# Kernel tuning notes

Hardware: AMD Instinct MI355X
Metric: run time of the kernel (lower is better)

Reference implementation:

```python
import jax, jax.numpy as jnp
import numpy as np

VOCAB, EMB, HID, B, T = 50000, 16, 32, 4096, 500


def setup_inputs() -> dict:
    key = jax.random.key(0)
    k1, k2, k3, k4 = jax.random.split(key, 4)
    tokens = jax.random.randint(k1, (B, T), 0, VOCAB, dtype=jnp.int32)
    emb_table = jax.random.normal(k2, (VOCAB, EMB), dtype=jnp.float32) * 0.05
    kernel = jax.random.normal(k3, (EMB, 4 * HID), dtype=jnp.float32) * (1.0 / np.sqrt(EMB))
    rec_kernel = jax.random.normal(k4, (HID, 4 * HID), dtype=jnp.float32) * (1.0 / np.sqrt(HID))
    # Keras default: unit_forget_bias=True -> forget-gate bias = 1
    bias = jnp.concatenate([
        jnp.zeros((HID,), jnp.float32),
        jnp.ones((HID,), jnp.float32),
        jnp.zeros((2 * HID,), jnp.float32),
    ])
    return {"tokens": tokens, "emb_table": emb_table, "kernel": kernel,
            "rec_kernel": rec_kernel, "bias": bias}


def reference(tokens, emb_table, kernel, rec_kernel, bias):
    # Embedding with mask_zero=True: mask = tokens != 0
    embedded = emb_table[tokens]                 # [B, T, EMB]
    mask = (tokens != 0)                         # [B, T] bool
    # Precompute input projections for all timesteps (one big GEMM)
    x_proj = jnp.einsum('bte,eh->bth', embedded, kernel) + bias  # [B, T, 4H]

    def step(carry, xs):
        h, c = carry                              # [B, H] each
        xp_t, m_t = xs                            # [B, 4H], [B]
        z = xp_t + h @ rec_kernel                 # [B, 4H]
        i, f, g, o = jnp.split(z, 4, axis=-1)     # Keras gate order i,f,c,o
        i = jax.nn.sigmoid(i)
        f = jax.nn.sigmoid(f)
        g = jnp.tanh(g)
        o = jax.nn.sigmoid(o)
        c_new = f * c + i * g
        h_new = o * jnp.tanh(c_new)
        m = m_t[:, None]
        # masked steps carry previous state through (Keras LSTM mask semantics)
        h = jnp.where(m, h_new, h)
        c = jnp.where(m, c_new, c)
        return (h, c), None

    h0 = jnp.zeros((tokens.shape[0], HID), jnp.float32)
    c0 = jnp.zeros((tokens.shape[0], HID), jnp.float32)
    xs = (jnp.swapaxes(x_proj, 0, 1), jnp.swapaxes(mask, 0, 1))  # time-major
    (h, c), _ = jax.lax.scan(step, (h0, c0), xs)
    return h                                      # [B, HID] last (masked) output
```

## Files before the change

kernel.cpp:

```cpp
#include <hip/hip_runtime.h>
#include <cstdint>

#define VOCAB_N 50000
#define EMB_N   16
#define HID_N   32
#define B_N     4096
#define T_N     500

typedef __attribute__((ext_vector_type(8))) short bf16x8;
typedef __attribute__((ext_vector_type(4))) float f32x4;

__device__ __forceinline__ float frcp(float x) { return __builtin_amdgcn_rcpf(x); }
__device__ __forceinline__ float sigm(float x) {
  return frcp(1.0f + exp2f(x * -1.4426950408889634f));
}
__device__ __forceinline__ float tanh_fast(float x) {
  return fmaf(-2.0f, frcp(1.0f + exp2f(x * 2.8853900817779268f)), 1.0f);
}

__device__ __forceinline__ unsigned bf16_split_pack(float x) {
  unsigned u  = __builtin_bit_cast(unsigned, x);
  float hif = __builtin_bit_cast(float, u & 0xFFFF0000u);
  float r   = x - hif;
  unsigned lo = __builtin_bit_cast(unsigned, r) >> 16;
  return (u >> 16) | (lo << 16);
}

__global__ void build_proj_mfma(const float* __restrict__ emb,
                                const float* __restrict__ W,
                                const float* __restrict__ bias,
                                float* __restrict__ proj) {
  __shared__ float Wl[EMB_N * 128];
  __shared__ float bl[128];
  const int tid = threadIdx.x;
  for (int i = tid; i < EMB_N * 128 / 4; i += 256)
    reinterpret_cast<float4*>(Wl)[i] = reinterpret_cast<const float4*>(W)[i];
  if (tid < 32)
    reinterpret_cast<float4*>(bl)[tid] = reinterpret_cast<const float4*>(bias)[tid];
  __syncthreads();

  const long long gid = (long long)blockIdx.x * 256 + tid;
  if (gid >= (long long)VOCAB_N * 128) return;
  const int v = (int)(gid >> 7);
  const int q = (int)(gid & 127);
  const int c = q >> 3, n = q & 7;
  const int col = n * 16 + c;

  const float4* ev = reinterpret_cast<const float4*>(emb + (size_t)v * EMB_N);
  float4 e0 = ev[0], e1 = ev[1], e2 = ev[2], e3 = ev[3];
  const float em[16] = {e0.x,e0.y,e0.z,e0.w, e1.x,e1.y,e1.z,e1.w,
                        e2.x,e2.y,e2.z,e2.w, e3.x,e3.y,e3.z,e3.w};
  float a = bl[col];
#pragma unroll
  for (int e = 0; e < EMB_N; ++e) a = fmaf(em[e], Wl[e * 128 + col], a);
  proj[gid] = a;
}

#define SPLIT8(VAL, IDX)                                                      \
  { unsigned s_ = bf16_split_pack(VAL);                                       \
    Ah[IDX] = (short)s_; Al[IDX] = (short)(s_ >> 16); }

#define LSTM_MSTEP(TOKC, TOKP, XP0, XP1)                                      \
  {                                                                           \
                \
    float4 hv0 = *reinterpret_cast<const float4*>(&hl[c16][g8]);              \
    float4 hv1 = *reinterpret_cast<const float4*>(&hl[c16][g8 + 4]);          \
    bf16x8 Ah, Al;                                                            \
    SPLIT8(hv0.x, 0) SPLIT8(hv0.y, 1) SPLIT8(hv0.z, 2) SPLIT8(hv0.w, 3)      \
    SPLIT8(hv1.x, 4) SPLIT8(hv1.y, 5) SPLIT8(hv1.z, 6) SPLIT8(hv1.w, 7)      \
    f32x4 z0 = {(XP0).x, 0.f, 0.f, 0.f};                                      \
    f32x4 z1 = {(XP0).y, 0.f, 0.f, 0.f};                                      \
    f32x4 z2 = {(XP0).z, 0.f, 0.f, 0.f};                                      \
    f32x4 z3 = {(XP0).w, 0.f, 0.f, 0.f};                                      \
    f32x4 z4 = {(XP1).x, 0.f, 0.f, 0.f};                                      \
    f32x4 z5 = {(XP1).y, 0.f, 0.f, 0.f};                                      \
    f32x4 z6 = {(XP1).z, 0.f, 0.f, 0.f};                                      \
    f32x4 z7 = {(XP1).w, 0.f, 0.f, 0.f};                                      \
    z0 = __builtin_amdgcn_mfma_f32_16x16x32_bf16(Ah, Bh0, z0, 0, 0, 0);       \
    z1 = __builtin_amdgcn_mfma_f32_16x16x32_bf16(Ah, Bh1, z1, 0, 0, 0);       \
    z2 = __builtin_amdgcn_mfma_f32_16x16x32_bf16(Ah, Bh2, z2, 0, 0, 0);       \
    z3 = __builtin_amdgcn_mfma_f32_16x16x32_bf16(Ah, Bh3, z3, 0, 0, 0);       \
    z4 = __builtin_amdgcn_mfma_f32_16x16x32_bf16(Ah, Bh4, z4, 0, 0, 0);       \
    z5 = __builtin_amdgcn_mfma_f32_16x16x32_bf16(Ah, Bh5, z5, 0, 0, 0);       \
    z6 = __builtin_amdgcn_mfma_f32_16x16x32_bf16(Ah, Bh6, z6, 0, 0, 0);       \
    z7 = __builtin_amdgcn_mfma_f32_16x16x32_bf16(Ah, Bh7, z7, 0, 0, 0);       \
    z0 = __builtin_amdgcn_mfma_f32_16x16x32_bf16(Ah, Bl0, z0, 0, 0, 0);       \
    z1 = __builtin_amdgcn_mfma_f32_16x16x32_bf16(Ah, Bl1, z1, 0, 0, 0);       \
    z2 = __builtin_amdgcn_mfma_f32_16x16x32_bf16(Ah, Bl2, z2, 0, 0, 0);       \
    z3 = __builtin_amdgcn_mfma_f32_16x16x32_bf16(Ah, Bl3, z3, 0, 0, 0);       \
    z4 = __builtin_amdgcn_mfma_f32_16x16x32_bf16(Ah, Bl4, z4, 0, 0, 0);       \
    z5 = __builtin_amdgcn_mfma_f32_16x16x32_bf16(Ah, Bl5, z5, 0, 0, 0);       \
    z6 = __builtin_amdgcn_mfma_f32_16x16x32_bf16(Ah, Bl6, z6, 0, 0, 0);       \
    z7 = __builtin_amdgcn_mfma_f32_16x16x32_bf16(Ah, Bl7, z7, 0, 0, 0);       \
    z0 = __builtin_amdgcn_mfma_f32_16x16x32_bf16(Al, Bh0, z0, 0, 0, 0);       \
    z1 = __builtin_amdgcn_mfma_f32_16x16x32_bf16(Al, Bh1, z1, 0, 0, 0);       \
    z2 = __builtin_amdgcn_mfma_f32_16x16x32_bf16(Al, Bh2, z2, 0, 0, 0);       \
    z3 = __builtin_amdgcn_mfma_f32_16x16x32_bf16(Al, Bh3, z3, 0, 0, 0);       \
    z4 = __builtin_amdgcn_mfma_f32_16x16x32_bf16(Al, Bh4, z4, 0, 0, 0);       \
    z5 = __builtin_amdgcn_mfma_f32_16x16x32_bf16(Al, Bh5, z5, 0, 0, 0);       \
    z6 = __builtin_amdgcn_mfma_f32_16x16x32_bf16(Al, Bh6, z6, 0, 0, 0);       \
    z7 = __builtin_amdgcn_mfma_f32_16x16x32_bf16(Al, Bh7, z7, 0, 0, 0);       \
                          \
    {                                                                         \
      const float4* xp_p = reinterpret_cast<const float4*>(                   \
          proj + ((size_t)(TOKP) << 7) + c16 * 8);                            \
      (XP0) = xp_p[0]; (XP1) = xp_p[1];                                       \
    }                                                                         \
                    \
    {                                                                         \
      float i0 = sigm(z0.x), f0 = sigm(z2.x);                                 \
      float g0 = tanh_fast(z4.x), o0 = sigm(z6.x);                            \
      float i1 = sigm(z1.x), f1 = sigm(z3.x);                                 \
      float g1 = tanh_fast(z5.x), o1 = sigm(z7.x);                            \
      float cn0 = fmaf(f0, c0, i0 * g0);                                      \
      float cn1 = fmaf(f1, c1, i1 * g1);                                      \
      float hn0 = o0 * tanh_fast(cn0);                                        \
      float hn1 = o1 * tanh_fast(cn1);                                        \
      bool m = (TOKC) != 0;                                                   \
      c0 = m ? cn0 : c0;  h0 = m ? hn0 : h0;                                  \
      c1 = m ? cn1 : c1;  h1 = m ? hn1 : h1;                                  \
      hl[myrow][c16]      = h0;                                               \
      hl[myrow][c16 + 16] = h1;                                               \
      asm volatile("" ::: "memory");      \
    }                                                                         \
  }

__global__ __launch_bounds__(64, 1)
void lstm_mfma_kernel(const int*   __restrict__ tokens,
                      const float* __restrict__ rec_kernel,
                      const float* __restrict__ proj,
                      float*       __restrict__ out) {
  __shared__ float hl[16][36];
  __shared__ int   tokl[4][512];

  const int l   = threadIdx.x;
  const int g   = l >> 4;
  const int c16 = l & 15;
  const int g8  = g * 8;
  const int myrow = 4 * g;

  for (int i = l; i < 16 * 36; i += 64) (&hl[0][0])[i] = 0.0f;

  {
    const int4* src = reinterpret_cast<const int4*>(tokens + (size_t)blockIdx.x * 4 * T_N);
    for (int i = l; i < T_N; i += 64) {
      int4 v4 = src[i];
      int gi = 4 * i;
      int r  = gi / T_N;
      int cc = gi - r * T_N;
      *reinterpret_cast<int4*>(&tokl[r][cc]) = v4;
    }
    if (l < 48) { int r = l / 12, cc = T_N + (l % 12); tokl[r][cc] = 0; }
  }
  asm volatile("" ::: "memory");

  bf16x8 Bh0, Bh1, Bh2, Bh3, Bh4, Bh5, Bh6, Bh7;
  bf16x8 Bl0, Bl1, Bl2, Bl3, Bl4, Bl5, Bl6, Bl7;
#define BUILD_B(N, BH, BL)                                                    \
  {                                                                           \
    _Pragma("unroll")                                                         \
    for (int j = 0; j < 8; ++j) {                                             \
      float x = rec_kernel[(g8 + j) * 128 + (N) * 16 + c16];                  \
      unsigned s_ = bf16_split_pack(x);                                       \
      (BH)[j] = (short)s_; (BL)[j] = (short)(s_ >> 16);                       \
    }                                                                         \
  }
  BUILD_B(0, Bh0, Bl0) BUILD_B(1, Bh1, Bl1) BUILD_B(2, Bh2, Bl2)
  BUILD_B(3, Bh3, Bl3) BUILD_B(4, Bh4, Bl4) BUILD_B(5, Bh5, Bl5)
  BUILD_B(6, Bh6, Bl6) BUILD_B(7, Bh7, Bl7)
#undef BUILD_B

  float c0 = 0.f, c1 = 0.f, h0 = 0.f, h1 = 0.f;

  int tA = tokl[g][0], tB = tokl[g][1], tC = tokl[g][2], tD = tokl[g][3];

  float4 xpA0, xpA1, xpB0, xpB1;
  {
    const float4* p0 = reinterpret_cast<const float4*>(proj + ((size_t)tA << 7) + c16 * 8);
    xpA0 = p0[0]; xpA1 = p0[1];
    const float4* p1 = reinterpret_cast<const float4*>(proj + ((size_t)tB << 7) + c16 * 8);
    xpB0 = p1[0]; xpB1 = p1[1];
  }

#pragma unroll 1
  for (int t = 0; t < T_N; t += 2) {
    int2 tnew = *reinterpret_cast<const int2*>(&tokl[g][t + 4]);

    LSTM_MSTEP(tA, tC, xpA0, xpA1);
    LSTM_MSTEP(tB, tD, xpB0, xpB1);

    tA = tC; tB = tD; tC = tnew.x; tD = tnew.y;
  }

  const size_t obase = ((size_t)blockIdx.x * 4 + g) * HID_N;
  out[obase + c16]      = h0;
  out[obase + c16 + 16] = h1;
}

__global__ __launch_bounds__(256, 2)
void lstm_scan_fallback(const int*   __restrict__ tokens,
                        const float* __restrict__ rec_kernel,
                        const float* __restrict__ emb,
                        const float* __restrict__ W,
                        const float* __restrict__ bias,
                        float*       __restrict__ out) {
  __shared__ int   tokl[8][T_N];
  __shared__ float hbuf[8][HID_N];

  const int tid  = threadIdx.x;
  const int wv   = tid >> 6;
  const int lane = tid & 63;
  const int half = lane >> 5;
  const int j    = lane & 31;
  const int wrow = wv * 2 + half;
  const int row  = blockIdx.x * 8 + wrow;

  {
    const int4* src = reinterpret_cast<const int4*>(tokens + (size_t)blockIdx.x * 8 * T_N);
    int4* dst = reinterpret_cast<int4*>(&tokl[0][0]);
    for (int i = tid; i < 8 * T_N / 4; i += 256) dst[i] = src[i];
  }

  float wr[HID_N][4];
#pragma unroll
  for (int k = 0; k < HID_N; ++k)
#pragma unroll
    for (int gg2 = 0; gg2 < 4; ++gg2) wr[k][gg2] = rec_kernel[k * 128 + gg2 * 32 + j];

  float wk[EMB_N][4];
  float bb[4];
#pragma unroll
  for (int e = 0; e < EMB_N; ++e)
#pragma unroll
    for (int gg2 = 0; gg2 < 4; ++gg2) wk[e][gg2] = W[e * 128 + gg2 * 32 + j];
#pragma unroll
  for (int gg2 = 0; gg2 < 4; ++gg2) bb[gg2] = bias[gg2 * 32 + j];
  __syncthreads();

  float c = 0.0f, h = 0.0f;
  float4 h4[8];
#pragma unroll
  for (int q = 0; q < 8; ++q) h4[q] = make_float4(0.f, 0.f, 0.f, 0.f);

  for (int t = 0; t < T_N; ++t) {
    const int tokc = tokl[wrow][t];
    const float4* ev = reinterpret_cast<const float4*>(emb + (size_t)tokc * EMB_N);
    float4 e0 = ev[0], e1 = ev[1], e2 = ev[2], e3 = ev[3];
    const float em[16] = {e0.x,e0.y,e0.z,e0.w, e1.x,e1.y,e1.z,e1.w,
                          e2.x,e2.y,e2.z,e2.w, e3.x,e3.y,e3.z,e3.w};
    float a0 = bb[0], a1 = bb[1], a2 = bb[2], a3 = bb[3];
#pragma unroll
    for (int e = 0; e < EMB_N; ++e) {
      float x = em[e];
      a0 = fmaf(x, wk[e][0], a0); a1 = fmaf(x, wk[e][1], a1);
      a2 = fmaf(x, wk[e][2], a2); a3 = fmaf(x, wk[e][3], a3);
    }
#pragma unroll
    for (int q = 0; q < 8; ++q) {
      float hx = h4[q].x, hy = h4[q].y, hz = h4[q].z, hw = h4[q].w;
      a0 = fmaf(hx, wr[4*q+0][0], a0); a1 = fmaf(hx, wr[4*q+0][1], a1);
      a2 = fmaf(hx, wr[4*q+0][2], a2); a3 = fmaf(hx, wr[4*q+0][3], a3);
      a0 = fmaf(hy, wr[4*q+1][0], a0); a1 = fmaf(hy, wr[4*q+1][1], a1);
      a2 = fmaf(hy, wr[4*q+1][2], a2); a3 = fmaf(hy, wr[4*q+1][3], a3);
      a0 = fmaf(hz, wr[4*q+2][0], a0); a1 = fmaf(hz, wr[4*q+2][1], a1);
      a2 = fmaf(hz, wr[4*q+2][2], a2); a3 = fmaf(hz, wr[4*q+2][3], a3);
      a0 = fmaf(hw, wr[4*q+3][0], a0); a1 = fmaf(hw, wr[4*q+3][1], a1);
      a2 = fmaf(hw, wr[4*q+3][2], a2); a3 = fmaf(hw, wr[4*q+3][3], a3);
    }
    float ig = sigm(a0), fg = sigm(a1), gg = tanh_fast(a2), og = sigm(a3);
    float cn = fmaf(fg, c, ig * gg);
    float hn = og * tanh_fast(cn);
    if (tokc != 0) { h = hn; c = cn; }
    hbuf[wrow][j] = h;
    asm volatile("" ::: "memory");
#pragma unroll
    for (int q = 0; q < 8; ++q)
      h4[q] = reinterpret_cast<const float4*>(&hbuf[wrow][0])[q];
    asm volatile("" ::: "memory");
  }
  out[(size_t)row * HID_N + j] = h;
}

extern "C" void kernel_launch(void* const* d_in, const int* in_sizes, int n_in,
                              void* d_out, int out_size, void* d_ws, size_t ws_size,
                              hipStream_t stream) {
  const int*   tokens = (const int*)  d_in[0];
  const float* emb    = (const float*)d_in[1];
  const float* W      = (const float*)d_in[2];
  const float* rec    = (const float*)d_in[3];
  const float* bias   = (const float*)d_in[4];
  float* out = (float*)d_out;

  const size_t need = (size_t)VOCAB_N * 128 * sizeof(float);
  if (ws_size >= need) {
    float* proj = (float*)d_ws;
    const long long total = (long long)VOCAB_N * 128;
    build_proj_mfma<<<(int)((total + 255) / 256), 256, 0, stream>>>(emb, W, bias, proj);
    lstm_mfma_kernel<<<B_N / 4, 64, 0, stream>>>(tokens, rec, proj, out);
  } else {
    lstm_scan_fallback<<<B_N / 8, 256, 0, stream>>>(tokens, rec, emb, W, bias, out);
  }
}
```

Measured before the change: 438.4 us.

## Restructure LSTM recurrence to use all MFMA output rows across two waves

Each block now processes 16 sequences with two wavefronts, each handling half of the gate columns, so all four rows of every MFMA accumulator carry real data instead of only one. The hidden state is stored in LDS as a pre-split bf16 hi/lo pair and double-buffered with a workgroup barrier per step. LOG2E is folded into the projection table and the recurrent weights to remove multiplies in the gate math. The per-step MFMA count per wave drops from 24 to 12, in exchange for a cross-wave barrier and more LDS traffic every step.

```diff
diff --git a/kernel.cpp b/kernel.cpp
--- a/kernel.cpp
+++ b/kernel.cpp
@@ -6,17 +6,14 @@
 #define HID_N   32
 #define B_N     4096
 #define T_N     500
+#define LOG2E     1.4426950408889634f
+#define TWOLOG2E  2.8853900817779268f
 
 typedef __attribute__((ext_vector_type(8))) short bf16x8;
 typedef __attribute__((ext_vector_type(4))) float f32x4;
+typedef __attribute__((ext_vector_type(4))) unsigned int u32x4;
 
 __device__ __forceinline__ float frcp(float x) { return __builtin_amdgcn_rcpf(x); }
-__device__ __forceinline__ float sigm(float x) {
-  return frcp(1.0f + exp2f(x * -1.4426950408889634f));
-}
-__device__ __forceinline__ float tanh_fast(float x) {
-  return fmaf(-2.0f, frcp(1.0f + exp2f(x * 2.8853900817779268f)), 1.0f);
-}
 
 __device__ __forceinline__ unsigned bf16_split_pack(float x) {
   unsigned u  = __builtin_bit_cast(unsigned, x);
@@ -25,11 +22,16 @@
   unsigned lo = __builtin_bit_cast(unsigned, r) >> 16;
   return (u >> 16) | (lo << 16);
 }
-
-__global__ void build_proj_mfma(const float* __restrict__ emb,
-                                const float* __restrict__ W,
-                                const float* __restrict__ bias,
-                                float* __restrict__ proj) {
+__device__ __forceinline__ float unpack_h(unsigned p) {
+  float hi = __builtin_bit_cast(float, p << 16);
+  float lo = __builtin_bit_cast(float, p & 0xFFFF0000u);
+  return hi + lo;
+}
+
+__global__ void build_proj_ns(const float* __restrict__ emb,
+                              const float* __restrict__ W,
+                              const float* __restrict__ bias,
+                              float* __restrict__ proj) {
   __shared__ float Wl[EMB_N * 128];
   __shared__ float bl[128];
   const int tid = threadIdx.x;
@@ -43,8 +45,10 @@
   if (gid >= (long long)VOCAB_N * 128) return;
   const int v = (int)(gid >> 7);
   const int q = (int)(gid & 127);
-  const int c = q >> 3, n = q & 7;
-  const int col = n * 16 + c;
+  const int c  = q >> 3;
+  const int par = (q >> 2) & 1;
+  const int n2 = q & 3;
+  const int col = (2 * n2 + par) * 16 + c;
 
   const float4* ev = reinterpret_cast<const float4*>(emb + (size_t)v * EMB_N);
   float4 e0 = ev[0], e1 = ev[1], e2 = ev[2], e3 = ev[3];
@@ -53,148 +57,166 @@
   float a = bl[col];
 #pragma unroll
   for (int e = 0; e < EMB_N; ++e) a = fmaf(em[e], Wl[e * 128 + col], a);
-  proj[gid] = a;
-}
-
-#define SPLIT8(VAL, IDX)                                                      \
-  { unsigned s_ = bf16_split_pack(VAL);                                       \
-    Ah[IDX] = (short)s_; Al[IDX] = (short)(s_ >> 16); }
-
-#define LSTM_MSTEP(TOKC, TOKP, XP0, XP1)                                      \
+  proj[gid] = a * LOG2E;
+}
+
+#define GATE(R, TOK, CC, HH)                                                  \
   {                                                                           \
-                \
-    float4 hv0 = *reinterpret_cast<const float4*>(&hl[c16][g8]);              \
-    float4 hv1 = *reinterpret_cast<const float4*>(&hl[c16][g8 + 4]);          \
-    bf16x8 Ah, Al;                                                            \
-    SPLIT8(hv0.x, 0) SPLIT8(hv0.y, 1) SPLIT8(hv0.z, 2) SPLIT8(hv0.w, 3)      \
-    SPLIT8(hv1.x, 4) SPLIT8(hv1.y, 5) SPLIT8(hv1.z, 6) SPLIT8(hv1.w, 7)      \
-    f32x4 z0 = {(XP0).x, 0.f, 0.f, 0.f};                                      \
-    f32x4 z1 = {(XP0).y, 0.f, 0.f, 0.f};                                      \
-    f32x4 z2 = {(XP0).z, 0.f, 0.f, 0.f};                                      \
-    f32x4 z3 = {(XP0).w, 0.f, 0.f, 0.f};                                      \
-    f32x4 z4 = {(XP1).x, 0.f, 0.f, 0.f};                                      \
-    f32x4 z5 = {(XP1).y, 0.f, 0.f, 0.f};                                      \
-    f32x4 z6 = {(XP1).z, 0.f, 0.f, 0.f};                                      \
-    f32x4 z7 = {(XP1).w, 0.f, 0.f, 0.f};                                      \
+    float zi = z0[R], zf = z1[R], zg = z2[R], zo = z3[R];                     \
+    float gi = frcp(1.0f + exp2f(-zi));                                       \
+    float gf = frcp(1.0f + exp2f(-zf));                                       \
+    float gg = fmaf(-2.0f, frcp(1.0f + exp2f(zg + zg)), 1.0f);                \
+    float go = frcp(1.0f + exp2f(-zo));                                       \
+    float cn = fmaf(gf, CC, gi * gg);                                         \
+    float tc = fmaf(-2.0f, frcp(1.0f + exp2f(cn * TWOLOG2E)), 1.0f);          \
+    float hn = go * tc;                                                       \
+    bool m = (TOK) != 0;                                                      \
+    CC = m ? cn : CC;                                                         \
+    unsigned hp_ = bf16_split_pack(hn);                                       \
+    HH = m ? hp_ : HH;                                                        \
+    hl[pp ^ 1][rb + (R)][unit] = HH;                                          \
+  }
+
+#define BODY(TM, TP, X0, X1, X2, X3, TT4)                                     \
+  {                                                                           \
+    const unsigned* hrow = &hl[pp][c16][g8];                                  \
+    u32x4 wa = *reinterpret_cast<const u32x4*>(hrow);                         \
+    u32x4 wb = *reinterpret_cast<const u32x4*>(hrow + 4);                     \
+    u32x4 ahp, alp;                                                           \
+    ahp[0] = __builtin_amdgcn_perm(wa[1], wa[0], 0x05040100u);                \
+    alp[0] = __builtin_amdgcn_perm(wa[1], wa[0], 0x07060302u);                \
+    ahp[1] = __builtin_amdgcn_perm(wa[3], wa[2], 0x05040100u);                \
+    alp[1] = __builtin_amdgcn_perm(wa[3], wa[2], 0x07060302u);                \
+    ahp[2] = __builtin_amdgcn_perm(wb[1], wb[0], 0x05040100u);                \
+    alp[2] = __builtin_amdgcn_perm(wb[1], wb[0], 0x07060302u);                \
+    ahp[3] = __builtin_amdgcn_perm(wb[3], wb[2], 0x05040100u);                \
+    alp[3] = __builtin_amdgcn_perm(wb[3], wb[2], 0x07060302u);                \
+    bf16x8 Ah = __builtin_bit_cast(bf16x8, ahp);                              \
+    bf16x8 Al = __builtin_bit_cast(bf16x8, alp);                              \
+    f32x4 z0 = {(X0).x, (X1).x, (X2).x, (X3).x};                              \
+    f32x4 z1 = {(X0).y, (X1).y, (X2).y, (X3).y};                              \
+    f32x4 z2 = {(X0).z, (X1).z, (X2).z, (X3).z};                              \
+    f32x4 z3 = {(X0).w, (X1).w, (X2).w, (X3).w};                              \
+    \
+    (X0) = *reinterpret_cast<const float4*>(projw + (size_t)(TP).x * 128);    \
+    (X1) = *reinterpret_cast<const float4*>(projw + (size_t)(TP).y * 128);    \
+    (X2) = *reinterpret_cast<const float4*>(projw + (size_t)(TP).z * 128);    \
+    (X3) = *reinterpret_cast<const float4*>(projw + (size_t)(TP).w * 128);    \
     z0 = __builtin_amdgcn_mfma_f32_16x16x32_bf16(Ah, Bh0, z0, 0, 0, 0);       \
     z1 = __builtin_amdgcn_mfma_f32_16x16x32_bf16(Ah, Bh1, z1, 0, 0, 0);       \
     z2 = __builtin_amdgcn_mfma_f32_16x16x32_bf16(Ah, Bh2, z2, 0, 0, 0);       \
     z3 = __builtin_amdgcn_mfma_f32_16x16x32_bf16(Ah, Bh3, z3, 0, 0, 0);       \
-    z4 = __builtin_amdgcn_mfma_f32_16x16x32_bf16(Ah, Bh4, z4, 0, 0, 0);       \
-    z5 = __builtin_amdgcn_mfma_f32_16x16x32_bf16(Ah, Bh5, z5, 0, 0, 0);       \
-    z6 = __builtin_amdgcn_mfma_f32_16x16x32_bf16(Ah, Bh6, z6, 0, 0, 0);       \
-    z7 = __builtin_amdgcn_mfma_f32_16x16x32_bf16(Ah, Bh7, z7, 0, 0, 0);       \
+    z0 = __builtin_amdgcn_mfma_f32_16x16x32_bf16(Al, Bh0, z0, 0, 0, 0);       \
+    z1 = __builtin_amdgcn_mfma_f32_16x16x32_bf16(Al, Bh1, z1, 0, 0, 0);       \
+    z2 = __builtin_amdgcn_mfma_f32_16x16x32_bf16(Al, Bh2, z2, 0, 0, 0);       \
+    z3 = __builtin_amdgcn_mfma_f32_16x16x32_bf16(Al, Bh3, z3, 0, 0, 0);       \
     z0 = __builtin_amdgcn_mfma_f32_16x16x32_bf16(Ah, Bl0, z0, 0, 0, 0);       \
     z1 = __builtin_amdgcn_mfma_f32_16x16x32_bf16(Ah, Bl1, z1, 0, 0, 0);       \
     z2 = __builtin_amdgcn_mfma_f32_16x16x32_bf16(Ah, Bl2, z2, 0, 0, 0);       \
     z3 = __builtin_amdgcn_mfma_f32_16x16x32_bf16(Ah, Bl3, z3, 0, 0, 0);       \
-    z4 = __builtin_amdgcn_mfma_f32_16x16x32_bf16(Ah, Bl4, z4, 0, 0, 0);       \
-    z5 = __builtin_amdgcn_mfma_f32_16x16x32_bf16(Ah, Bl5, z5, 0, 0, 0);       \
-    z6 = __builtin_amdgcn_mfma_f32_16x16x32_bf16(Ah, Bl6, z6, 0, 0, 0);       \
-    z7 = __builtin_amdgcn_mfma_f32_16x16x32_bf16(Ah, Bl7, z7, 0, 0, 0);       \
-    z0 = __builtin_amdgcn_mfma_f32_16x16x32_bf16(Al, Bh0, z0, 0, 0, 0);       \
-    z1 = __builtin_amdgcn_mfma_f32_16x16x32_bf16(Al, Bh1, z1, 0, 0, 0);       \
-    z2 = __builtin_amdgcn_mfma_f32_16x16x32_bf16(Al, Bh2, z2, 0, 0, 0);       \
-    z3 = __builtin_amdgcn_mfma_f32_16x16x32_bf16(Al, Bh3, z3, 0, 0, 0);       \
-    z4 = __builtin_amdgcn_mfma_f32_16x16x32_bf16(Al, Bh4, z4, 0, 0, 0);       \
-    z5 = __builtin_amdgcn_mfma_f32_16x16x32_bf16(Al, Bh5, z5, 0, 0, 0);       \
-    z6 = __builtin_amdgcn_mfma_f32_16x16x32_bf16(Al, Bh6, z6, 0, 0, 0);       \
-    z7 = __builtin_amdgcn_mfma_f32_16x16x32_bf16(Al, Bh7, z7, 0, 0, 0);       \
-                          \
-    {                                                                         \
-      const float4* xp_p = reinterpret_cast<const float4*>(                   \
-          proj + ((size_t)(TOKP) << 7) + c16 * 8);                            \
-      (XP0) = xp_p[0]; (XP1) = xp_p[1];                                       \
-    }                                                                         \
-                    \
-    {                                                                         \
-      float i0 = sigm(z0.x), f0 = sigm(z2.x);                                 \
-      float g0 = tanh_fast(z4.x), o0 = sigm(z6.x);                            \
-      float i1 = sigm(z1.x), f1 = sigm(z3.x);                                 \
-      float g1 = tanh_fast(z5.x), o1 = sigm(z7.x);                            \
-      float cn0 = fmaf(f0, c0, i0 * g0);                                      \
-      float cn1 = fmaf(f1, c1, i1 * g1);                                      \
-      float hn0 = o0 * tanh_fast(cn0);                                        \
-      float hn1 = o1 * tanh_fast(cn1);                                        \
-      bool m = (TOKC) != 0;                                                   \
-      c0 = m ? cn0 : c0;  h0 = m ? hn0 : h0;                                  \
-      c1 = m ? cn1 : c1;  h1 = m ? hn1 : h1;                                  \
-      hl[myrow][c16]      = h0;                                               \
-      hl[myrow][c16 + 16] = h1;                                               \
-      asm volatile("" ::: "memory");      \
-    }                                                                         \
-  }
-
-__global__ __launch_bounds__(64, 1)
-void lstm_mfma_kernel(const int*   __restrict__ tokens,
-                      const float* __restrict__ rec_kernel,
-                      const float* __restrict__ proj,
-                      float*       __restrict__ out) {
-  __shared__ float hl[16][36];
-  __shared__ int   tokl[4][512];
-
-  const int l   = threadIdx.x;
+                                                  \
+    int4 tnew = make_int4(tokl[rb + 0][TT4], tokl[rb + 1][TT4],               \
+                          tokl[rb + 2][TT4], tokl[rb + 3][TT4]);              \
+    GATE(0, (TM).x, c0, hr0)                                                  \
+    GATE(1, (TM).y, c1, hr1)                                                  \
+    GATE(2, (TM).z, c2, hr2)                                                  \
+    GATE(3, (TM).w, c3, hr3)                                                  \
+    asm volatile("s_waitcnt lgkmcnt(0)" ::: "memory");                        \
+    __builtin_amdgcn_s_barrier();                                             \
+    asm volatile("" ::: "memory");                                            \
+    __builtin_amdgcn_sched_barrier(0);                                        \
+    pp ^= 1;                                                                  \
+    (TM) = (TP); (TP) = tnew;                                                 \
+  }
+
+__global__ __launch_bounds__(128, 1)
+void lstm_mfma_ns(const int*   __restrict__ tokens,
+                  const float* __restrict__ rec_kernel,
+                  const float* __restrict__ proj,
+                  float*       __restrict__ out) {
+  __shared__ int      tokl[16][512];
+  __shared__ unsigned hl[2][16][36];
+
+  const int tid = threadIdx.x;
+  const int wv  = tid >> 6;
+  const int l   = tid & 63;
+  const int c16 = l & 15;
   const int g   = l >> 4;
-  const int c16 = l & 15;
   const int g8  = g * 8;
-  const int myrow = 4 * g;
-
-  for (int i = l; i < 16 * 36; i += 64) (&hl[0][0])[i] = 0.0f;
+  const int rb  = g * 4;
+  const int unit = wv * 16 + c16;
 
   {
-    const int4* src = reinterpret_cast<const int4*>(tokens + (size_t)blockIdx.x * 4 * T_N);
-    for (int i = l; i < T_N; i += 64) {
+    const int4* src = reinterpret_cast<const int4*>(tokens + (size_t)blockIdx.x * 16 * T_N);
+    for (int i = tid; i < 16 * T_N / 4; i += 128) {
       int4 v4 = src[i];
       int gi = 4 * i;
       int r  = gi / T_N;
       int cc = gi - r * T_N;
       *reinterpret_cast<int4*>(&tokl[r][cc]) = v4;
     }
-    if (l < 48) { int r = l / 12, cc = T_N + (l % 12); tokl[r][cc] = 0; }
-  }
-  asm volatile("" ::: "memory");
-
-  bf16x8 Bh0, Bh1, Bh2, Bh3, Bh4, Bh5, Bh6, Bh7;
-  bf16x8 Bl0, Bl1, Bl2, Bl3, Bl4, Bl5, Bl6, Bl7;
-#define BUILD_B(N, BH, BL)                                                    \
+    for (int i = tid; i < 16 * 12; i += 128) {
+      int r = i / 12; tokl[r][T_N + (i % 12)] = 0;
+    }
+  }
+
+  hl[0][rb + 0][unit] = 0; hl[0][rb + 1][unit] = 0;
+  hl[0][rb + 2][unit] = 0; hl[0][rb + 3][unit] = 0;
+
+  bf16x8 Bh0, Bh1, Bh2, Bh3, Bl0, Bl1, Bl2, Bl3;
+#define BUILD_B(Q, BH, BL)                                                    \
   {                                                                           \
     _Pragma("unroll")                                                         \
     for (int j = 0; j < 8; ++j) {                                             \
-      float x = rec_kernel[(g8 + j) * 128 + (N) * 16 + c16];                  \
+      float x = rec_kernel[(g8 + j) * 128 + (2 * (Q) + wv) * 16 + c16] * LOG2E;\
       unsigned s_ = bf16_split_pack(x);                                       \
       (BH)[j] = (short)s_; (BL)[j] = (short)(s_ >> 16);                       \
     }                                                                         \
   }
-  BUILD_B(0, Bh0, Bl0) BUILD_B(1, Bh1, Bl1) BUILD_B(2, Bh2, Bl2)
-  BUILD_B(3, Bh3, Bl3) BUILD_B(4, Bh4, Bl4) BUILD_B(5, Bh5, Bl5)
-  BUILD_B(6, Bh6, Bl6) BUILD_B(7, Bh7, Bl7)
+  BUILD_B(0, Bh0, Bl0) BUILD_B(1, Bh1, Bl1)
+  BUILD_B(2, Bh2, Bl2) BUILD_B(3, Bh3, Bl3)
 #undef BUILD_B
 
-  float c0 = 0.f, c1 = 0.f, h0 = 0.f, h1 = 0.f;
-
-  int tA = tokl[g][0], tB = tokl[g][1], tC = tokl[g][2], tD = tokl[g][3];
-
-  float4 xpA0, xpA1, xpB0, xpB1;
-  {
-    const float4* p0 = reinterpret_cast<const float4*>(proj + ((size_t)tA << 7) + c16 * 8);
-    xpA0 = p0[0]; xpA1 = p0[1];
-    const float4* p1 = reinterpret_cast<const float4*>(proj + ((size_t)tB << 7) + c16 * 8);
-    xpB0 = p1[0]; xpB1 = p1[1];
-  }
+  __syncthreads();
+
+  float    c0 = 0.f, c1 = 0.f, c2 = 0.f, c3 = 0.f;
+  unsigned hr0 = 0, hr1 = 0, hr2 = 0, hr3 = 0;
+  int pp = 0;
+
+  int4 tmA = make_int4(tokl[rb+0][0], tokl[rb+1][0], tokl[rb+2][0], tokl[rb+3][0]);
+  int4 tmB = make_int4(tokl[rb+0][1], tokl[rb+1][1], tokl[rb+2][1], tokl[rb+3][1]);
+  int4 tpA = make_int4(tokl[rb+0][2], tokl[rb+1][2], tokl[rb+2][2], tokl[rb+3][2]);
+  int4 tpB = make_int4(tokl[rb+0][3], tokl[rb+1][3], tokl[rb+2][3], tokl[rb+3][3]);
+
+  const float* projw = proj + c16 * 8 + wv * 4;
+  float4 xA0 = *reinterpret_cast<const float4*>(projw + (size_t)tmA.x * 128);
+  float4 xA1 = *reinterpret_cast<const float4*>(projw + (size_t)tmA.y * 128);
+  float4 xA2 = *reinterpret_cast<const float4*>(projw + (size_t)tmA.z * 128);
+  float4 xA3 = *reinterpret_cast<const float4*>(projw + (size_t)tmA.w * 128);
+  float4 xB0 = *reinterpret_cast<const float4*>(projw + (size_t)tmB.x * 128);
+  float4 xB1 = *reinterpret_cast<const float4*>(projw + (size_t)tmB.y * 128);
+  float4 xB2 = *reinterpret_cast<const float4*>(projw + (size_t)tmB.z * 128);
+  float4 xB3 = *reinterpret_cast<const float4*>(projw + (size_t)tmB.w * 128);
 
 #pragma unroll 1
   for (int t = 0; t < T_N; t += 2) {
-    int2 tnew = *reinterpret_cast<const int2*>(&tokl[g][t + 4]);
-
-    LSTM_MSTEP(tA, tC, xpA0, xpA1);
-    LSTM_MSTEP(tB, tD, xpB0, xpB1);
-
-    tA = tC; tB = tD; tC = tnew.x; tD = tnew.y;
-  }
-
-  const size_t obase = ((size_t)blockIdx.x * 4 + g) * HID_N;
-  out[obase + c16]      = h0;
-  out[obase + c16 + 16] = h1;
+    BODY(tmA, tpA, xA0, xA1, xA2, xA3, t + 4);
+    BODY(tmB, tpB, xB0, xB1, xB2, xB3, t + 5);
+  }
+
+  const size_t obase = (size_t)blockIdx.x * 16 + rb;
+  out[(obase + 0) * HID_N + unit] = unpack_h(hr0);
+  out[(obase + 1) * HID_N + unit] = unpack_h(hr1);
+  out[(obase + 2) * HID_N + unit] = unpack_h(hr2);
+  out[(obase + 3) * HID_N + unit] = unpack_h(hr3);
+}
+
+__device__ __forceinline__ float sigm_fb(float x) {
+  return frcp(1.0f + exp2f(x * -1.4426950408889634f));
+}
+__device__ __forceinline__ float tanh_fb(float x) {
+  float e = exp2f(x * 2.8853900817779268f);
+  return fmaf(-2.0f, frcp(e + 1.0f), 1.0f);
 }
 
 __global__ __launch_bounds__(256, 2)
@@ -267,9 +289,9 @@
       a0 = fmaf(hw, wr[4*q+3][0], a0); a1 = fmaf(hw, wr[4*q+3][1], a1);
       a2 = fmaf(hw, wr[4*q+3][2], a2); a3 = fmaf(hw, wr[4*q+3][3], a3);
     }
-    float ig = sigm(a0), fg = sigm(a1), gg = tanh_fast(a2), og = sigm(a3);
+    float ig = sigm_fb(a0), fg = sigm_fb(a1), gg = tanh_fb(a2), og = sigm_fb(a3);
     float cn = fmaf(fg, c, ig * gg);
-    float hn = og * tanh_fast(cn);
+    float hn = og * tanh_fb(cn);
     if (tokc != 0) { h = hn; c = cn; }
     hbuf[wrow][j] = h;
     asm volatile("" ::: "memory");
@@ -295,8 +317,8 @@
   if (ws_size >= need) {
     float* proj = (float*)d_ws;
     const long long total = (long long)VOCAB_N * 128;
-    build_proj_mfma<<<(int)((total + 255) / 256), 256, 0, stream>>>(emb, W, bias, proj);
-    lstm_mfma_kernel<<<B_N / 4, 64, 0, stream>>>(tokens, rec, proj, out);
+    build_proj_ns<<<(int)((total + 255) / 256), 256, 0, stream>>>(emb, W, bias, proj);
+    lstm_mfma_ns<<<B_N / 16, 128, 0, stream>>>(tokens, rec, proj, out);
   } else {
     lstm_scan_fallback<<<B_N / 8, 256, 0, stream>>>(tokens, rec, emb, W, bias, out);
   }
```

After: 392.9 us. 1.12x faster.
